# Kernel optimization log

Hardware: AMD Instinct MI355X
Metric: run time of the kernel (lower is better)

## Reference

```python
import jax, jax.numpy as jnp
import numpy as np

N_NODES = 50000
N_EDGES = 1200000
N_OD = 10000
D_NODE = 16
D_EDGE = 8
HID = 64
N_LAYERS = 3
K_MIN = 1.0
K_MAX = 50.0


def setup_inputs() -> dict:
    key = jax.random.key(0)
    ks = jax.random.split(key, 24)
    s = 0.05
    inp = {
        "node_features": jax.random.normal(ks[0], (N_NODES, D_NODE), jnp.float32),
        "edge_index": jax.random.randint(ks[1], (2, N_EDGES), 0, N_NODES, jnp.int32),
        "edge_features": jax.random.normal(ks[2], (N_EDGES, D_EDGE), jnp.float32),
        "od_pairs": jax.random.randint(ks[3], (2, N_OD), 0, N_NODES, jnp.int32),
        "traffic_stats": jax.random.normal(ks[4], (4,), jnp.float32),
        # projections
        "Wn": jax.random.normal(ks[5], (D_NODE, HID), jnp.float32) * s,
        "bn": jnp.zeros((HID,), jnp.float32),
        "We": jax.random.normal(ks[6], (D_EDGE, HID), jnp.float32) * s,
        "be": jnp.zeros((HID,), jnp.float32),
        # stacked GNN layer weights: message MLP on [h_src, e], update MLP on [h, agg]
        "Wm": jax.random.normal(ks[7], (N_LAYERS, 2 * HID, HID), jnp.float32) * s,
        "bm": jnp.zeros((N_LAYERS, HID), jnp.float32),
        "Wu": jax.random.normal(ks[8], (N_LAYERS, 2 * HID, HID), jnp.float32) * s,
        "bu": jnp.zeros((N_LAYERS, HID), jnp.float32),
        # per-flow score MLP on [h_src, h_dst]
        "Ws1": jax.random.normal(ks[9], (2 * HID, HID), jnp.float32) * s,
        "bs1": jnp.zeros((HID,), jnp.float32),
        "Ws2": jax.random.normal(ks[10], (HID, 1), jnp.float32) * s,
        "bs2": jnp.zeros((1,), jnp.float32),
        # DynamicKHead: Linear(HID+4,32) -> ReLU -> Linear(32,16) -> ReLU -> Linear(16,1)
        "Wk1": jax.random.normal(ks[11], (HID + 4, 32), jnp.float32) * s,
        "bk1": jnp.zeros((32,), jnp.float32),
        "Wk2": jax.random.normal(ks[12], (32, 16), jnp.float32) * s,
        "bk2": jnp.zeros((16,), jnp.float32),
        "Wk3": jax.random.normal(ks[13], (16, 1), jnp.float32) * s,
        "bk3": jnp.zeros((1,), jnp.float32),
    }
    return inp


def _forward(node_features, edge_features, traffic_stats,
             Wn, bn, We, be, Wm, bm, Wu, bu,
             Ws1, bs1, Ws2, bs2, Wk1, bk1, Wk2, bk2, Wk3, bk3,
             edge_index, od_pairs):
    relu = jax.nn.relu
    h = relu(node_features @ Wn + bn)          # [N, HID]
    e = relu(edge_features @ We + be)          # [E, HID]
    src, dst = edge_index[0], edge_index[1]
    for l in range(N_LAYERS):
        # gather-compute-scatter message passing with edge features
        m = relu(jnp.concatenate([h[src], e], axis=-1) @ Wm[l] + bm[l])  # [E, HID]
        agg = jax.ops.segment_sum(m, dst, num_segments=N_NODES)          # [N, HID]
        h = relu(jnp.concatenate([h, agg], axis=-1) @ Wu[l] + bu[l]) + h  # residual
    # per-flow scores from OD endpoint embeddings
    hp = jnp.concatenate([h[od_pairs[0]], h[od_pairs[1]]], axis=-1)      # [P, 2*HID]
    scores = (relu(hp @ Ws1 + bs1) @ Ws2 + bs2).squeeze(-1)              # [P]
    # dynamic-K head (dropout = identity in eval)
    graph_embed = h.mean(axis=0)                                          # [HID]
    x = jnp.concatenate([graph_embed, traffic_stats], axis=-1)
    raw = (relu(relu(x @ Wk1 + bk1) @ Wk2 + bk2) @ Wk3 + bk3).squeeze(-1)
    k_continuous = K_MIN + jax.nn.sigmoid(raw) * (K_MAX - K_MIN)
    return scores, k_continuous


def reference(node_features, edge_index, edge_features, od_pairs, traffic_stats,
              Wn, bn, We, be, Wm, bm, Wu, bu,
              Ws1, bs1, Ws2, bs2, Wk1, bk1, Wk2, bk2, Wk3, bk3):
    return _forward(node_features, edge_features, traffic_stats,
                    Wn, bn, We, be, Wm, bm, Wu, bu,
                    Ws1, bs1, Ws2, bs2, Wk1, bk1, Wk2, bk2, Wk3, bk3,
                    edge_index, od_pairs)
```

## Files before the change

kernel.cpp:

```cpp
#include <hip/hip_runtime.h>
#include <hip/hip_bf16.h>

#define OFF_WN   0
#define OFF_BN   1024
#define OFF_WE   1088
#define OFF_BE   1600
#define OFF_WM   1664
#define OFF_BM   26240
#define OFF_WU   26432
#define OFF_BU   51008
#define OFF_WS1  51200
#define OFF_BS1  59392
#define OFF_WS2  59456
#define OFF_BS2  59520
#define OFF_WK1  59521
#define OFF_BK1  61697
#define OFF_WK2  61729
#define OFF_BK2  62241
#define OFF_WK3  62257
#define OFF_BK3  62273
#define OFF_TS   62274
#define OFF_GSUM 62278
#define OFF_FLAG 62344
#define OFF_BSUM 62400
#define OFF_BOFF 62900
#define OFF_H    65536

typedef __attribute__((ext_vector_type(8))) short bfrag;
typedef __attribute__((ext_vector_type(4))) float ffrag;

__device__ __forceinline__ float bf2f(unsigned short u) {
    unsigned int i = ((unsigned int)u) << 16;
    float f;
    __builtin_memcpy(&f, &i, sizeof(f));
    return f;
}
__device__ __forceinline__ float bflo(unsigned int u) {
    unsigned int i = u << 16;
    float f; __builtin_memcpy(&f, &i, sizeof(f)); return f;
}
__device__ __forceinline__ float bfhi(unsigned int u) {
    unsigned int i = u & 0xffff0000u;
    float f; __builtin_memcpy(&f, &i, sizeof(f)); return f;
}
__device__ __forceinline__ unsigned int f2bf_rne(float f) {
    unsigned int u; __builtin_memcpy(&u, &f, 4);
    return (u + 0x7fffu + ((u >> 16) & 1u)) >> 16;
}
__device__ __forceinline__ unsigned int pack2bf(float a, float b) {
    return f2bf_rne(a) | (f2bf_rne(b) << 16);
}
__device__ __forceinline__ unsigned int cvt_pk_bf16(float a, float b) {
    unsigned int r;
    asm("v_cvt_pk_bf16_f32 %0, %1, %2" : "=v"(r) : "v"(a), "v"(b));
    return r;
}

__global__ void detect_dtype_kernel(const unsigned short* __restrict__ nf,
                                    int* __restrict__ flag) {
    int t = threadIdx.x;
    float m = 0.f;
    for (int i = t; i < 1024; i += 64) {
        float v = fabsf(bf2f(nf[i]));
        if (!isnan(v)) m = fmaxf(m, v);
        else m = 1e30f;
    }
    for (int o = 32; o > 0; o >>= 1) m = fmaxf(m, __shfl_down(m, o));
    if (t == 0) flag[0] = (m > 1e6f) ? 1 : 0;
}

struct ConvArgs {
    const void* src[19];
    int off[19];
    int n[19];
};

__global__ __launch_bounds__(256) void convert_all_kernel(
        ConvArgs a, float* __restrict__ ws, const int* __restrict__ flagp) {
    int isf32 = *flagp;
    int ai = blockIdx.y;
    int i  = blockIdx.x * blockDim.x + threadIdx.x;
    if (i < a.n[ai]) {
        float v = isf32 ? ((const float*)a.src[ai])[i]
                        : bf2f(((const unsigned short*)a.src[ai])[i]);
        ws[a.off[ai] + i] = v;
    }
}

__global__ __launch_bounds__(256) void wtrans_prep_kernel(
        const float* __restrict__ ws, short* __restrict__ Wb) {
    int idx = blockIdx.x * 256 + threadIdx.x;
    if (idx < 12288) {
        int l = idx >> 12, rem = idx & 4095, n = rem >> 6, k = rem & 63;
        Wb[idx] = (short)f2bf_rne(ws[OFF_WM + l * 8192 + 4096 + k * 64 + n]);
    } else if (idx < 24576) {
        int j = idx - 12288;
        int l = j >> 12, rem = j & 4095, n = rem >> 6, k = rem & 63;
        Wb[idx] = (short)f2bf_rne(ws[OFF_WM + l * 8192 + k * 64 + n]);
    } else if (idx < 49152) {
        int j = idx - 24576;
        int l = j >> 13, rem = j & 8191, n = rem >> 7, k = rem & 127;
        Wb[idx] = (short)f2bf_rne(ws[OFF_WU + l * 8192 + k * 64 + n]);
    } else if (idx < 51200) {
        int j = idx - 49152;
        int n = j >> 5, k = j & 31;
        Wb[idx] = (k < 8) ? (short)f2bf_rne(ws[OFF_WE + k * 64 + n]) : (short)0;
    } else if (idx < 59392) {
        int j = idx - 51200;
        int n = j >> 7, k = j & 127;
        Wb[idx] = (short)f2bf_rne(ws[OFF_WS1 + k * 64 + n]);
    }
}

__global__ __launch_bounds__(256) void node_proj_kernel(
        const void* __restrict__ nf, const float* __restrict__ ws,
        float* __restrict__ h, int N, const int* __restrict__ flagp) {
    int idx = blockIdx.x * blockDim.x + threadIdx.x;
    if (idx >= N * 64) return;
    int isf32 = *flagp;
    int i = idx >> 6, c = idx & 63;
    const float* Wn = ws + OFF_WN;
    float acc = ws[OFF_BN + c];
    float x[16];
    if (isf32) {
        const float* row = (const float*)nf + (size_t)i * 16;
#pragma unroll
        for (int k = 0; k < 16; ++k) x[k] = row[k];
    } else {
        const unsigned short* row = (const unsigned short*)nf + (size_t)i * 16;
#pragma unroll
        for (int k = 0; k < 16; ++k) x[k] = bf2f(row[k]);
    }
#pragma unroll
    for (int k = 0; k < 16; ++k) acc = fmaf(x[k], Wn[k * 64 + c], acc);
    h[idx] = fmaxf(acc, 0.f);
}

__global__ __launch_bounds__(256) void count_kernel(
        const int* __restrict__ dst, int* __restrict__ deg,
        int* __restrict__ rank, int E, int dorank) {
    int e = blockIdx.x * blockDim.x + threadIdx.x;
    if (e < E) {
        int r = atomicAdd(&deg[dst[e]], 1);
        if (dorank) rank[e] = r;
    }
}

__global__ __launch_bounds__(256) void scan_blocks_kernel(
        const int* __restrict__ deg, int* __restrict__ incl,
        int* __restrict__ bsum, int N) {
    int tid = threadIdx.x;
    int gid = blockIdx.x * 256 + tid;
    int v = (gid < N) ? deg[gid] : 0;
    int lane = tid & 63, w = tid >> 6;
    int x = v;
#pragma unroll
    for (int o = 1; o < 64; o <<= 1) {
        int y = __shfl_up(x, o);
        if (lane >= o) x += y;
    }
    __shared__ int wsum[4];
    __shared__ int woff[4];
    if (lane == 63) wsum[w] = x;
    __syncthreads();
    if (tid == 0) {
        int a = 0;
#pragma unroll
        for (int i = 0; i < 4; ++i) { woff[i] = a; a += wsum[i]; }
    }
    __syncthreads();
    x += woff[w];
    if (gid < N) incl[gid] = x;
    if (tid == 255) bsum[blockIdx.x] = x;
}

__global__ __launch_bounds__(256) void scan_bsum_kernel(
        const int* __restrict__ bsum, int* __restrict__ boff, int nb) {
    __shared__ int sh[256];
    int tid = threadIdx.x;
    int carry = 0;
    for (int base = 0; base < nb; base += 256) {
        int v = (base + tid < nb) ? bsum[base + tid] : 0;
        sh[tid] = v;
        __syncthreads();
        for (int o = 1; o < 256; o <<= 1) {
            int t = (tid >= o) ? sh[tid - o] : 0;
            __syncthreads();
            sh[tid] += t;
            __syncthreads();
        }
        if (base + tid < nb) boff[base + tid] = carry + sh[tid] - v;
        __syncthreads();
        carry += sh[255];
        __syncthreads();
    }
}

__global__ __launch_bounds__(256) void scan_finalize_kernel(
        const int* __restrict__ deg, const int* __restrict__ incl,
        const int* __restrict__ boff, int* __restrict__ out,
        int* __restrict__ cursor, int N, int tailval) {
    int gid = blockIdx.x * 256 + threadIdx.x;
    if (gid < N) {
        int ex = boff[blockIdx.x] + incl[gid] - deg[gid];
        out[gid] = ex;
        cursor[gid] = ex;
    }
    if (gid == 0) out[N] = tailval;
}

__global__ __launch_bounds__(256) void fill_kernel(
        const int* __restrict__ src, const int* __restrict__ dst,
        const void* __restrict__ ef, int* __restrict__ cursor,
        const int* __restrict__ rank, const int* __restrict__ off,
        int* __restrict__ eid, int* __restrict__ srcs,
        float* __restrict__ rec, int E, int big,
        const int* __restrict__ flagp) {
    int e = blockIdx.x * blockDim.x + threadIdx.x;
    if (e >= E) return;
    int d = dst[e];
    if (big) {
        int pos = off[d] + rank[e];
        unsigned p01, p23, p45, p67;
        if (*flagp) {
            const float4* p = (const float4*)ef + (size_t)e * 2;
            float4 a = p[0], b = p[1];
            p01 = pack2bf(a.x, a.y); p23 = pack2bf(a.z, a.w);
            p45 = pack2bf(b.x, b.y); p67 = pack2bf(b.z, b.w);
        } else {
            uint4 r = ((const uint4*)ef)[e];
            p01 = r.x; p23 = r.y; p45 = r.z; p67 = r.w;
        }
        float* o = rec + (size_t)pos * 6;
        *(uint2*)o       = make_uint2((unsigned)src[e], (unsigned)d);
        *(uint2*)(o + 2) = make_uint2(p01, p23);
        *(uint2*)(o + 4) = make_uint2(p45, p67);
    } else {
        int pos = atomicAdd(&cursor[d], 1);
        eid[pos] = e;
        srcs[pos] = src[e];
    }
}

__global__ __launch_bounds__(256) void spans_kernel(
        const int* __restrict__ off, int* __restrict__ spans, int N) {
    int i = blockIdx.x * blockDim.x + threadIdx.x;
    if (i >= N) return;
    int k0 = off[i], k1 = off[i + 1];
    spans[i] = (k1 > k0) ? (((k1 - 1) >> 6) - (k0 >> 6) + 1) : 0;
}

__global__ __launch_bounds__(256) void nodeA_mfma_kernel(
        const short* __restrict__ W1T, const float* __restrict__ bm,
        const float* __restrict__ h, float* __restrict__ A, int N) {
    __shared__ short lds_w[64 * 72];
    __shared__ short lds_x[4][64 * 72];
    const int tid = threadIdx.x, wid = tid >> 6, lane = tid & 63;
    const int r = lane & 15, q = lane >> 4;
    const int nb0 = blockIdx.x * 256 + wid * 64;

#pragma unroll
    for (int j = 0; j < 2; ++j) {
        int f8 = (tid * 2 + j) * 8;
        int row = f8 >> 6, k = f8 & 63;
        *(uint4*)&lds_w[row * 72 + k] = ((const uint4*)W1T)[tid * 2 + j];
    }
    short* xt = &lds_x[wid][0];
#pragma unroll 1
    for (int it = 0; it < 16; ++it) {
        int f4 = it * 64 + lane;
        int node = f4 >> 4, c4 = f4 & 15;
        int gn = nb0 + node; if (gn >= N) gn = N - 1;
        float4 v = ((const float4*)h)[(size_t)gn * 16 + c4];
        *(uint2*)&xt[node * 72 + c4 * 4] =
            make_uint2(pack2bf(v.x, v.y), pack2bf(v.z, v.w));
    }
    __syncthreads();

    bfrag bg[4][2];
#pragma unroll
    for (int ni = 0; ni < 4; ++ni)
#pragma unroll
        for (int ki = 0; ki < 2; ++ki)
            bg[ni][ki] = *(const bfrag*)&lds_w[(ni * 16 + r) * 72 + ki * 32 + q * 8];
    float buv[4];
#pragma unroll
    for (int ni = 0; ni < 4; ++ni) buv[ni] = bm[ni * 16 + r];

    ffrag C[4][4];
#pragma unroll
    for (int mi = 0; mi < 4; ++mi) {
        bfrag af[2];
#pragma unroll
        for (int ki = 0; ki < 2; ++ki)
            af[ki] = *(const bfrag*)&xt[(mi * 16 + r) * 72 + ki * 32 + q * 8];
#pragma unroll
        for (int ni = 0; ni < 4; ++ni) {
            ffrag c = {buv[ni], buv[ni], buv[ni], buv[ni]};
            c = __builtin_amdgcn_mfma_f32_16x16x32_bf16(af[0], bg[ni][0], c, 0, 0, 0);
            c = __builtin_amdgcn_mfma_f32_16x16x32_bf16(af[1], bg[ni][1], c, 0, 0, 0);
            C[mi][ni] = c;
        }
    }
#pragma unroll
    for (int mi = 0; mi < 4; ++mi)
#pragma unroll
        for (int rr = 0; rr < 4; ++rr) {
            int gn = nb0 + mi * 16 + q * 4 + rr;
            if (gn < N) {
#pragma unroll
                for (int ni = 0; ni < 4; ++ni)
                    A[(size_t)gn * 64 + ni * 16 + r] = C[mi][ni][rr];
            }
        }
}

__global__ __launch_bounds__(256, 4) void msg_mfma_red(
        const short* __restrict__ WeT, const float* __restrict__ be,
        const short* __restrict__ WbT, const float* __restrict__ rec,
        const float* __restrict__ A, float* __restrict__ pbuf,
        const int* __restrict__ off, const int* __restrict__ pstart, int E) {
    __shared__ short lds_ev[4][64 * 72];
    __shared__ int   lds_src[4][64];
    const int tid = threadIdx.x;
    const int wid = tid >> 6, lane = tid & 63;
    const int w = blockIdx.x * 4 + wid;
    if (w * 64 >= E) return;
    const int slot = w * 64 + lane;
    const int slotc = (slot < E) ? slot : (E - 1);

    const float* rbase = rec + (size_t)slotc * 6;
    uint2 u0 = *(const uint2*)rbase;
    uint2 u1 = *(const uint2*)(rbase + 2);
    uint2 u2 = *(const uint2*)(rbase + 4);
    int s  = (int)u0.x;
    int di = (int)u0.y;
    int pstv = pstart[di];
    int offv = off[di];
    lds_src[wid][lane] = s;

    short* evb = &lds_ev[wid][0];
    short* evrow = evb + lane * 72;
    *(uint4*)(evrow) = make_uint4(u1.x, u1.y, u2.x, u2.y);
    uint4 z4 = make_uint4(0u, 0u, 0u, 0u);
    *(uint4*)(evrow + 8)  = z4;
    *(uint4*)(evrow + 16) = z4;
    *(uint4*)(evrow + 24) = z4;

    const int r = lane & 15, q = lane >> 4;

    bfrag afe[4];
#pragma unroll
    for (int mi = 0; mi < 4; ++mi)
        afe[mi] = *(const bfrag*)(evb + (mi * 16 + r) * 72 + q * 8);

#pragma unroll
    for (int ni = 0; ni < 4; ++ni) {
        bfrag bge = *(const bfrag*)(WeT + (ni * 16 + r) * 32 + q * 8);
        float4 b4 = *(const float4*)(be + ni * 16 + q * 4);
#pragma unroll
        for (int mi = 0; mi < 4; ++mi) {
            ffrag c = {b4.x, b4.y, b4.z, b4.w};
            c = __builtin_amdgcn_mfma_f32_16x16x32_bf16(bge, afe[mi], c, 0, 0, 0);
            unsigned lo = cvt_pk_bf16(fmaxf(c[0], 0.f), fmaxf(c[1], 0.f));
            unsigned hi = cvt_pk_bf16(fmaxf(c[2], 0.f), fmaxf(c[3], 0.f));
            *(uint2*)(evb + (mi * 16 + r) * 72 + ni * 16 + q * 4) =
                make_uint2(lo, hi);
        }
    }

    bfrag af[4][2];
#pragma unroll
    for (int mi = 0; mi < 4; ++mi)
#pragma unroll
        for (int ki = 0; ki < 2; ++ki)
            af[mi][ki] = *(const bfrag*)(evb + (mi * 16 + r) * 72 + ki * 32 + q * 8);

    const float* ap[4][4];
#pragma unroll
    for (int mi = 0; mi < 4; ++mi) {
        int4 sr = *(const int4*)&lds_src[wid][mi * 16 + q * 4];
        ap[mi][0] = A + (size_t)sr.x * 64 + r;
        ap[mi][1] = A + (size_t)sr.y * 64 + r;
        ap[mi][2] = A + (size_t)sr.z * 64 + r;
        ap[mi][3] = A + (size_t)sr.w * 64 + r;
    }

#pragma unroll
    for (int ni = 0; ni < 4; ++ni) {
        bfrag bg0 = *(const bfrag*)(WbT + (ni * 16 + r) * 64 + q * 8);
        bfrag bg1 = *(const bfrag*)(WbT + (ni * 16 + r) * 64 + 32 + q * 8);
        ffrag C[4];
#pragma unroll
        for (int mi = 0; mi < 4; ++mi) {
            C[mi][0] = ap[mi][0][ni * 16];
            C[mi][1] = ap[mi][1][ni * 16];
            C[mi][2] = ap[mi][2][ni * 16];
            C[mi][3] = ap[mi][3][ni * 16];
        }
#pragma unroll
        for (int mi = 0; mi < 4; ++mi) {
            C[mi] = __builtin_amdgcn_mfma_f32_16x16x32_bf16(af[mi][0], bg0, C[mi], 0, 0, 0);
            C[mi] = __builtin_amdgcn_mfma_f32_16x16x32_bf16(af[mi][1], bg1, C[mi], 0, 0, 0);
        }
#pragma unroll
        for (int mi = 0; mi < 4; ++mi) {
            unsigned lo = cvt_pk_bf16(fmaxf(C[mi][0], 0.f), fmaxf(C[mi][1], 0.f));
            unsigned hi = cvt_pk_bf16(fmaxf(C[mi][2], 0.f), fmaxf(C[mi][3], 0.f));
            *(uint2*)(evb + (ni * 16 + r) * 72 + mi * 16 + q * 4) =
                make_uint2(lo, hi);
        }
    }

    int kmax = E - w * 64; if (kmax > 64) kmax = 64;
    if (kmax < 64) {
        for (int k = kmax; k < 64; ++k) evb[lane * 72 + k] = 0;
    }
    int prevd = __shfl_up(di, 1);
    unsigned long long sm = __ballot(lane != 0 && di != prevd);
    int curp = __shfl(pstv, 0) + (w - (__shfl(offv, 0) >> 6));
    float acc = 0.f;
#pragma unroll
    for (int g = 0; g < 8; ++g) {
        uint4 v = *(const uint4*)(evb + lane * 72 + g * 8);
        float f0 = bflo(v.x), f1 = bfhi(v.x), f2 = bflo(v.y), f3 = bfhi(v.y);
        float f4 = bflo(v.z), f5 = bfhi(v.z), f6 = bflo(v.w), f7 = bfhi(v.w);
        unsigned gm = (unsigned)(sm >> (g * 8)) & 0xffu;
        if (gm == 0) {
            acc += (((f0 + f1) + (f2 + f3)) + ((f4 + f5) + (f6 + f7)));
        } else {
            float fv[8] = {f0, f1, f2, f3, f4, f5, f6, f7};
#pragma unroll
            for (int j = 0; j < 8; ++j) {
                if (gm & (1u << j)) {
                    pbuf[(size_t)curp * 64 + lane] = acc;
                    acc = 0.f;
                    curp = __shfl(pstv, g * 8 + j);
                }
                acc += fv[j];
            }
        }
    }
    pbuf[(size_t)curp * 64 + lane] = acc;
}

__global__ __launch_bounds__(256) void fixup_kernel(
        const float* __restrict__ pbuf, const int* __restrict__ off,
        const int* __restrict__ pstart, float* __restrict__ agg, int N) {
    int tid = blockIdx.x * blockDim.x + threadIdx.x;
    int i = tid >> 2, q = tid & 3;
    if (i >= N) return;
    int k0 = off[i], k1 = off[i + 1];
    float acc[16];
#pragma unroll
    for (int c = 0; c < 16; ++c) acc[c] = 0.f;
    if (k1 > k0) {
        int nsp = ((k1 - 1) >> 6) - (k0 >> 6) + 1;
        int p = pstart[i];
        for (int j = 0; j < nsp; ++j) {
            const float4* pr = (const float4*)(pbuf + (size_t)(p + j) * 64 + q * 16);
#pragma unroll
            for (int c = 0; c < 4; ++c) {
                float4 v = pr[c];
                acc[4 * c] += v.x; acc[4 * c + 1] += v.y;
                acc[4 * c + 2] += v.z; acc[4 * c + 3] += v.w;
            }
        }
    }
    float4* o4 = (float4*)(agg + (size_t)i * 64 + q * 16);
#pragma unroll
    for (int c = 0; c < 4; ++c)
        o4[c] = make_float4(acc[4 * c], acc[4 * c + 1], acc[4 * c + 2], acc[4 * c + 3]);
}

__global__ __launch_bounds__(128) void update_mfma_kernel(
        const short* __restrict__ WuT, const float* __restrict__ bu,
        float* __restrict__ h, const float* __restrict__ agg, int N) {
    __shared__ short lds_w[64 * 136];
    __shared__ short lds_x[2][64 * 136];
    const int tid = threadIdx.x, wid = tid >> 6, lane = tid & 63;
    const int r = lane & 15, q = lane >> 4;
    const int nb0 = blockIdx.x * 128 + wid * 64;
#pragma unroll
    for (int j = 0; j < 8; ++j) {
        int f8 = (tid * 8 + j) * 8;
        int row = f8 >> 7, k = f8 & 127;
        *(uint4*)&lds_w[row * 136 + k] = ((const uint4*)WuT)[tid * 8 + j];
    }
    short* xt = &lds_x[wid][0];
#pragma unroll 1
    for (int it = 0; it < 32; ++it) {
        int f4 = it * 64 + lane;
        int node = f4 >> 5, c4 = f4 & 31;
        int gn = nb0 + node; if (gn >= N) gn = N - 1;
        const float4* src = (c4 < 16)
            ? ((const float4*)h + (size_t)gn * 16 + c4)
            : ((const float4*)agg + (size_t)gn * 16 + (c4 - 16));
        float4 v = *src;
        *(uint2*)&xt[node * 136 + c4 * 4] =
            make_uint2(pack2bf(v.x, v.y), pack2bf(v.z, v.w));
    }
    __syncthreads();
    bfrag bg[4][4];
#pragma unroll
    for (int ni = 0; ni < 4; ++ni)
#pragma unroll
        for (int ki = 0; ki < 4; ++ki)
            bg[ni][ki] = *(const bfrag*)&lds_w[(ni * 16 + r) * 136 + ki * 32 + q * 8];
    float buv[4];
#pragma unroll
    for (int ni = 0; ni < 4; ++ni) buv[ni] = bu[ni * 16 + r];
    ffrag C[4][4];
#pragma unroll
    for (int mi = 0; mi < 4; ++mi) {
        bfrag af[4];
#pragma unroll
        for (int ki = 0; ki < 4; ++ki)
            af[ki] = *(const bfrag*)&xt[(mi * 16 + r) * 136 + ki * 32 + q * 8];
#pragma unroll
        for (int ni = 0; ni < 4; ++ni) {
            ffrag c = {buv[ni], buv[ni], buv[ni], buv[ni]};
#pragma unroll
            for (int ki = 0; ki < 4; ++ki)
                c = __builtin_amdgcn_mfma_f32_16x16x32_bf16(af[ki], bg[ni][ki], c, 0, 0, 0);
            C[mi][ni] = c;
        }
    }
#pragma unroll
    for (int mi = 0; mi < 4; ++mi)
#pragma unroll
        for (int rr = 0; rr < 4; ++rr) {
            int nl = mi * 16 + q * 4 + rr;
            int gn = nb0 + nl;
            if (gn < N) {
#pragma unroll
                for (int ni = 0; ni < 4; ++ni) {
                    float hold = bf2f((unsigned short)xt[nl * 136 + ni * 16 + r]);
                    h[(size_t)gn * 64 + ni * 16 + r] =
                        fmaxf(C[mi][ni][rr], 0.f) + hold;
                }
            }
        }
}

__global__ __launch_bounds__(256) void gather_msg_fallback(
        const float* __restrict__ Wm2, const float* __restrict__ We,
        const float* __restrict__ be, const void* __restrict__ ef,
        const int* __restrict__ srcs, const int* __restrict__ eid,
        const int* __restrict__ off, const float* __restrict__ A,
        float* __restrict__ agg, int N, const int* __restrict__ flagp) {
    int i = blockIdx.x * blockDim.x + threadIdx.x;
    if (i >= N) return;
    int isf32 = *flagp;
    int k0 = off[i], k1 = off[i + 1];
    float acc[64];
#pragma unroll
    for (int c = 0; c < 64; ++c) acc[c] = 0.f;
    for (int k = k0; k < k1; ++k) {
        int s = srcs[k];
        int e = eid[k];
        const float4* a4 = (const float4*)(A + (size_t)s * 64);
        float t[64];
#pragma unroll
        for (int c = 0; c < 16; ++c) {
            float4 v = a4[c];
            t[4 * c] = v.x; t[4 * c + 1] = v.y; t[4 * c + 2] = v.z; t[4 * c + 3] = v.w;
        }
        float efv[8];
        if (isf32) {
            const float4* e4 = (const float4*)ef + (size_t)e * 2;
            float4 ra = e4[0], rb = e4[1];
            efv[0]=ra.x; efv[1]=ra.y; efv[2]=ra.z; efv[3]=ra.w;
            efv[4]=rb.x; efv[5]=rb.y; efv[6]=rb.z; efv[7]=rb.w;
        } else {
            uint4 rr = ((const uint4*)ef)[e];
            efv[0]=bflo(rr.x); efv[1]=bfhi(rr.x); efv[2]=bflo(rr.y); efv[3]=bfhi(rr.y);
            efv[4]=bflo(rr.z); efv[5]=bfhi(rr.z); efv[6]=bflo(rr.w); efv[7]=bfhi(rr.w);
        }
#pragma unroll 1
        for (int d0 = 0; d0 < 64; d0 += 8) {
            float ev[8];
#pragma unroll
            for (int dd = 0; dd < 8; ++dd) {
                float a = be[d0 + dd];
#pragma unroll
                for (int kk = 0; kk < 8; ++kk) a = fmaf(efv[kk], We[kk * 64 + d0 + dd], a);
                ev[dd] = fmaxf(a, 0.f);
            }
#pragma unroll
            for (int dd = 0; dd < 8; ++dd) {
                const float* w = Wm2 + (d0 + dd) * 64;
#pragma unroll
                for (int c = 0; c < 64; ++c) t[c] = fmaf(ev[dd], w[c], t[c]);
            }
        }
#pragma unroll
        for (int c = 0; c < 64; ++c) acc[c] += fmaxf(t[c], 0.f);
    }
    float4* o4 = (float4*)(agg + (size_t)i * 64);
#pragma unroll
    for (int c = 0; c < 16; ++c)
        o4[c] = make_float4(acc[4 * c], acc[4 * c + 1], acc[4 * c + 2], acc[4 * c + 3]);
}

__global__ __launch_bounds__(128) void scores_mfma_kernel(
        const short* __restrict__ Ws1T, const float* __restrict__ bs1,
        const float* __restrict__ Ws2, const float* __restrict__ bs2,
        const int* __restrict__ ods, const int* __restrict__ odd,
        const float* __restrict__ h, void* __restrict__ out, int P,
        const int* __restrict__ flagp) {
    __shared__ short lds_w[64 * 136];
    __shared__ short lds_x[2][64 * 136];
    const int tid = threadIdx.x, wid = tid >> 6, lane = tid & 63;
    const int r = lane & 15, q = lane >> 4;
    const int pb0 = blockIdx.x * 128 + wid * 64;
#pragma unroll
    for (int j = 0; j < 8; ++j) {
        int f8 = (tid * 8 + j) * 8;
        int row = f8 >> 7, k = f8 & 127;
        *(uint4*)&lds_w[row * 136 + k] = ((const uint4*)Ws1T)[tid * 8 + j];
    }
    short* xt = &lds_x[wid][0];
#pragma unroll 1
    for (int it = 0; it < 32; ++it) {
        int f4 = it * 64 + lane;
        int pr = f4 >> 5, c4 = f4 & 31;
        int gp = pb0 + pr; if (gp >= P) gp = P - 1;
        int node = (c4 < 16) ? ods[gp] : odd[gp];
        int cc = (c4 < 16) ? c4 : (c4 - 16);
        float4 v = ((const float4*)h)[(size_t)node * 16 + cc];
        *(uint2*)&xt[pr * 136 + c4 * 4] =
            make_uint2(pack2bf(v.x, v.y), pack2bf(v.z, v.w));
    }
    __syncthreads();

    bfrag bg[4][4];
#pragma unroll
    for (int ni = 0; ni < 4; ++ni)
#pragma unroll
        for (int ki = 0; ki < 4; ++ki)
            bg[ni][ki] = *(const bfrag*)&lds_w[(ni * 16 + r) * 136 + ki * 32 + q * 8];
    float buv[4], w2v[4];
#pragma unroll
    for (int ni = 0; ni < 4; ++ni) { buv[ni] = bs1[ni * 16 + r]; w2v[ni] = Ws2[ni * 16 + r]; }
    int isf32 = *flagp;
    float b2 = bs2[0];

#pragma unroll
    for (int mi = 0; mi < 4; ++mi) {
        bfrag af[4];
#pragma unroll
        for (int ki = 0; ki < 4; ++ki)
            af[ki] = *(const bfrag*)&xt[(mi * 16 + r) * 136 + ki * 32 + q * 8];
        float part[4] = {0.f, 0.f, 0.f, 0.f};
#pragma unroll
        for (int ni = 0; ni < 4; ++ni) {
            ffrag c = {buv[ni], buv[ni], buv[ni], buv[ni]};
#pragma unroll
            for (int ki = 0; ki < 4; ++ki)
                c = __builtin_amdgcn_mfma_f32_16x16x32_bf16(af[ki], bg[ni][ki], c, 0, 0, 0);
#pragma unroll
            for (int rr = 0; rr < 4; ++rr)
                part[rr] = fmaf(fmaxf(c[rr], 0.f), w2v[ni], part[rr]);
        }
#pragma unroll
        for (int rr = 0; rr < 4; ++rr) {
            float v = part[rr];
            v += __shfl_xor(v, 1); v += __shfl_xor(v, 2);
            v += __shfl_xor(v, 4); v += __shfl_xor(v, 8);
            if (r == 0) {
                int p = pb0 + mi * 16 + q * 4 + rr;
                if (p < P) {
                    float score = v + b2;
                    if (isf32) ((float*)out)[p] = score;
                    else ((__hip_bfloat16*)out)[p] = __float2bfloat16(score);
                }
            }
        }
    }
}

__global__ __launch_bounds__(256) void embed_kernel(
        const float* __restrict__ h, float* __restrict__ gsum, int N) {
    __shared__ float red[256];
    int c = threadIdx.x & 63;
    int sub = threadIdx.x >> 6;
    float a = 0.f;
    for (int i = blockIdx.x * 4 + sub; i < N; i += gridDim.x * 4)
        a += h[(size_t)i * 64 + c];
    red[threadIdx.x] = a;
    __syncthreads();
    if (threadIdx.x < 64) {
        float t = red[threadIdx.x] + red[threadIdx.x + 64] +
                  red[threadIdx.x + 128] + red[threadIdx.x + 192];
        unsafeAtomicAdd(&gsum[threadIdx.x], t);
    }
}

__global__ void khead_kernel(const float* __restrict__ ws,
                             void* __restrict__ out, int N, int P,
                             const int* __restrict__ flagp) {
    if (threadIdx.x != 0 || blockIdx.x != 0) return;
    float x[68];
    float invN = 1.f / (float)N;
#pragma unroll
    for (int c = 0; c < 64; ++c) x[c] = ws[OFF_GSUM + c] * invN;
#pragma unroll
    for (int k = 0; k < 4; ++k) x[64 + k] = ws[OFF_TS + k];
    float h1[32];
    for (int j = 0; j < 32; ++j) {
        float a = ws[OFF_BK1 + j];
        for (int i = 0; i < 68; ++i) a = fmaf(x[i], ws[OFF_WK1 + i * 32 + j], a);
        h1[j] = fmaxf(a, 0.f);
    }
    float h2[16];
    for (int k2 = 0; k2 < 16; ++k2) {
        float a = ws[OFF_BK2 + k2];
        for (int j = 0; j < 32; ++j) a = fmaf(h1[j], ws[OFF_WK2 + j * 16 + k2], a);
        h2[k2] = fmaxf(a, 0.f);
    }
    float raw = ws[OFF_BK3];
    for (int k2 = 0; k2 < 16; ++k2) raw = fmaf(h2[k2], ws[OFF_WK3 + k2], raw);
    float sig = 1.f / (1.f + expf(-raw));
    float k = 1.f + 49.f * sig;
    if (*flagp) ((float*)out)[P] = k;
    else ((__hip_bfloat16*)out)[P] = __float2bfloat16(k);
}

extern "C" void kernel_launch(void* const* d_in, const int* in_sizes, int n_in,
                              void* d_out, int out_size, void* d_ws, size_t ws_size,
                              hipStream_t stream) {
    const void* nf = d_in[0];
    const int*  ei = (const int*)d_in[1];
    const void* ef = d_in[2];
    const int*  od = (const int*)d_in[3];
    float* ws = (float*)d_ws;

    const int N = in_sizes[0] / 16;
    const int E = in_sizes[1] / 2;
    const int P = in_sizes[3] / 2;

    float* h      = ws + OFF_H;
    float* agg    = h + (size_t)N * 64;
    float* A      = agg + (size_t)N * 64;
    int*   deg    = (int*)(A + (size_t)N * 64);
    int*   off    = deg + N;
    int*   cursor = off + N + 1;
    int*   pstart = cursor + N;
    int*   eid    = pstart + N + 1;
    int*   srcs   = eid + E;
    short* WbT    = (short*)(srcs + E);
    short* W1T    = WbT + 12288;
    short* WuT    = WbT + 24576;
    short* WeT    = WbT + 49152;
    short* Ws1T   = WbT + 51200;
    int*   rank   = (int*)(WbT + 59392);
    int*   flag   = (int*)(ws + OFF_FLAG);
    int*   bsum   = (int*)(ws + OFF_BSUM);
    int*   boff   = (int*)(ws + OFF_BOFF);

    size_t fsofar = (size_t)OFF_H + 3 * (size_t)N * 64
                  + (size_t)(N + (N + 1) + N + (N + 1) + E + E + E) + 29696;
    size_t recOff = (fsofar + 7) & ~(size_t)7;
    float* rec = ws + recOff;
    size_t pbufOff = recOff + (size_t)E * 6;
    float* pbuf = ws + pbufOff;
    long pbufRows = (long)N + E / 64 + 128;
    size_t needBytes = (pbufOff + (size_t)pbufRows * 64) * sizeof(float);
    const bool big = (ws_size >= needBytes);

    const int* srcv = ei;
    const int* dstv = ei + E;

    detect_dtype_kernel<<<1, 64, 0, stream>>>((const unsigned short*)nf, flag);

    ConvArgs ca;
    const int srcidx[19] = {5, 6, 7, 8, 9, 10, 11, 12, 13, 14, 15, 16, 17, 18, 19, 20, 21, 22, 4};
    const int wsoff[19]  = {OFF_WN, OFF_BN, OFF_WE, OFF_BE, OFF_WM, OFF_BM, OFF_WU, OFF_BU,
                            OFF_WS1, OFF_BS1, OFF_WS2, OFF_BS2, OFF_WK1, OFF_BK1, OFF_WK2,
                            OFF_BK2, OFF_WK3, OFF_BK3, OFF_TS};
    int maxn = 0;
    for (int i = 0; i < 19; ++i) {
        ca.src[i] = d_in[srcidx[i]];
        ca.off[i] = wsoff[i];
        ca.n[i]   = in_sizes[srcidx[i]];
        if (ca.n[i] > maxn) maxn = ca.n[i];
    }
    dim3 cgrid((maxn + 255) / 256, 19);
    convert_all_kernel<<<cgrid, 256, 0, stream>>>(ca, ws, flag);
    wtrans_prep_kernel<<<232, 256, 0, stream>>>(ws, WbT);

    node_proj_kernel<<<(N * 64 + 255) / 256, 256, 0, stream>>>(nf, ws, h, N, flag);

    hipMemsetAsync(deg, 0, (size_t)N * sizeof(int), stream);
    count_kernel<<<(E + 255) / 256, 256, 0, stream>>>(dstv, deg, rank, E, big ? 1 : 0);
    int nb = (N + 255) / 256;
    scan_blocks_kernel<<<nb, 256, 0, stream>>>(deg, cursor, bsum, N);
    scan_bsum_kernel<<<1, 256, 0, stream>>>(bsum, boff, nb);
    scan_finalize_kernel<<<nb, 256, 0, stream>>>(deg, cursor, boff, off, cursor, N, E);
    fill_kernel<<<(E + 255) / 256, 256, 0, stream>>>(
        srcv, dstv, ef, cursor, rank, off, eid, srcs, rec, E, big ? 1 : 0, flag);

    if (big) {
        spans_kernel<<<nb, 256, 0, stream>>>(off, deg, N);
        scan_blocks_kernel<<<nb, 256, 0, stream>>>(deg, cursor, bsum, N);
        scan_bsum_kernel<<<1, 256, 0, stream>>>(bsum, boff, nb);
        scan_finalize_kernel<<<nb, 256, 0, stream>>>(deg, cursor, boff, pstart, cursor, N, 0);
    }

    const int N4 = N * 4;
    const int mblocks = (E + 255) / 256;
    const int ablocks = (N + 255) / 256;
    const int ublocks = (N + 127) / 128;
    for (int l = 0; l < 3; ++l) {
        nodeA_mfma_kernel<<<ablocks, 256, 0, stream>>>(
            W1T + l * 4096, ws + OFF_BM + l * 64, h, A, N);
        if (big) {
            msg_mfma_red<<<mblocks, 256, 0, stream>>>(
                WeT, ws + OFF_BE, WbT + l * 4096, rec, A, pbuf, off, pstart, E);
            fixup_kernel<<<(N4 + 255) / 256, 256, 0, stream>>>(
                pbuf, off, pstart, agg, N);
        } else {
            const float* Wm2 = ws + OFF_WM + l * 8192 + 4096;
            gather_msg_fallback<<<(N + 255) / 256, 256, 0, stream>>>(
                Wm2, ws + OFF_WE, ws + OFF_BE, ef, srcs, eid, off, A, agg, N, flag);
        }
        update_mfma_kernel<<<ublocks, 128, 0, stream>>>(
            WuT + l * 8192, ws + OFF_BU + l * 64, h, agg, N);
    }

    scores_mfma_kernel<<<(P + 127) / 128, 128, 0, stream>>>(
        Ws1T, ws + OFF_BS1, ws + OFF_WS2, ws + OFF_BS2,
        od, od + P, h, d_out, P, flag);

    hipMemsetAsync(ws + OFF_GSUM, 0, 64 * sizeof(float), stream);
    embed_kernel<<<256, 256, 0, stream>>>(h, ws + OFF_GSUM, N);
    khead_kernel<<<1, 64, 0, stream>>>(ws, d_out, N, P, flag);
}
```

Measured before the change: 621.8 us.

## Replace sorted edge records with index pairs and gather edge features in message kernel

The fill kernel now writes only an (edge id, src) pair per sorted slot, and a separate kernel converts edge features to bf16 in original edge order. The message kernel then gathers dst and the edge features through the edge id instead of reading a contiguous 24-byte sorted record. This makes the one-time scatter in fill cheaper, but each of the three layers now does random gathers of dst and 16-byte features. The khead kernel is also parallelised across a wavefront instead of running on a single thread.

```diff
diff --git a/kernel.cpp b/kernel.cpp
--- a/kernel.cpp
+++ b/kernel.cpp
@@ -211,35 +211,38 @@
 
 __global__ __launch_bounds__(256) void fill_kernel(
         const int* __restrict__ src, const int* __restrict__ dst,
-        const void* __restrict__ ef, int* __restrict__ cursor,
+        int* __restrict__ cursor,
         const int* __restrict__ rank, const int* __restrict__ off,
         int* __restrict__ eid, int* __restrict__ srcs,
-        float* __restrict__ rec, int E, int big,
-        const int* __restrict__ flagp) {
+        uint2* __restrict__ esb, int E, int big) {
     int e = blockIdx.x * blockDim.x + threadIdx.x;
     if (e >= E) return;
     int d = dst[e];
     if (big) {
         int pos = off[d] + rank[e];
-        unsigned p01, p23, p45, p67;
-        if (*flagp) {
-            const float4* p = (const float4*)ef + (size_t)e * 2;
-            float4 a = p[0], b = p[1];
-            p01 = pack2bf(a.x, a.y); p23 = pack2bf(a.z, a.w);
-            p45 = pack2bf(b.x, b.y); p67 = pack2bf(b.z, b.w);
-        } else {
-            uint4 r = ((const uint4*)ef)[e];
-            p01 = r.x; p23 = r.y; p45 = r.z; p67 = r.w;
-        }
-        float* o = rec + (size_t)pos * 6;
-        *(uint2*)o       = make_uint2((unsigned)src[e], (unsigned)d);
-        *(uint2*)(o + 2) = make_uint2(p01, p23);
-        *(uint2*)(o + 4) = make_uint2(p45, p67);
+        esb[pos] = make_uint2((unsigned)e, (unsigned)src[e]);
     } else {
         int pos = atomicAdd(&cursor[d], 1);
         eid[pos] = e;
         srcs[pos] = src[e];
     }
+}
+
+__global__ __launch_bounds__(256) void efb_kernel(
+        const void* __restrict__ ef, uint4* __restrict__ efb, int E,
+        const int* __restrict__ flagp) {
+    int e = blockIdx.x * blockDim.x + threadIdx.x;
+    if (e >= E) return;
+    uint4 v;
+    if (*flagp) {
+        const float4* p = (const float4*)ef + (size_t)e * 2;
+        float4 a = p[0], b = p[1];
+        v = make_uint4(pack2bf(a.x, a.y), pack2bf(a.z, a.w),
+                       pack2bf(b.x, b.y), pack2bf(b.z, b.w));
+    } else {
+        v = ((const uint4*)ef)[e];
+    }
+    efb[e] = v;
 }
 
 __global__ __launch_bounds__(256) void spans_kernel(
@@ -317,7 +320,8 @@
 
 __global__ __launch_bounds__(256, 4) void msg_mfma_red(
         const short* __restrict__ WeT, const float* __restrict__ be,
-        const short* __restrict__ WbT, const float* __restrict__ rec,
+        const short* __restrict__ WbT, const uint2* __restrict__ esb,
+        const int* __restrict__ dstv, const uint4* __restrict__ efb,
         const float* __restrict__ A, float* __restrict__ pbuf,
         const int* __restrict__ off, const int* __restrict__ pstart, int E) {
     __shared__ short lds_ev[4][64 * 72];
@@ -329,19 +333,17 @@
     const int slot = w * 64 + lane;
     const int slotc = (slot < E) ? slot : (E - 1);
 
-    const float* rbase = rec + (size_t)slotc * 6;
-    uint2 u0 = *(const uint2*)rbase;
-    uint2 u1 = *(const uint2*)(rbase + 2);
-    uint2 u2 = *(const uint2*)(rbase + 4);
-    int s  = (int)u0.x;
-    int di = (int)u0.y;
+    uint2 es = esb[slotc];
+    int e  = (int)es.x;
+    int s  = (int)es.y;
+    int di = dstv[e];
     int pstv = pstart[di];
     int offv = off[di];
     lds_src[wid][lane] = s;
 
     short* evb = &lds_ev[wid][0];
     short* evrow = evb + lane * 72;
-    *(uint4*)(evrow) = make_uint4(u1.x, u1.y, u2.x, u2.y);
+    *(uint4*)(evrow) = efb[e];
     uint4 z4 = make_uint4(0u, 0u, 0u, 0u);
     *(uint4*)(evrow + 8)  = z4;
     *(uint4*)(evrow + 16) = z4;
@@ -700,31 +702,34 @@
 __global__ void khead_kernel(const float* __restrict__ ws,
                              void* __restrict__ out, int N, int P,
                              const int* __restrict__ flagp) {
-    if (threadIdx.x != 0 || blockIdx.x != 0) return;
-    float x[68];
+    __shared__ float sh1[32];
+    __shared__ float sh2[16];
+    int lane = threadIdx.x;
     float invN = 1.f / (float)N;
-#pragma unroll
-    for (int c = 0; c < 64; ++c) x[c] = ws[OFF_GSUM + c] * invN;
-#pragma unroll
-    for (int k = 0; k < 4; ++k) x[64 + k] = ws[OFF_TS + k];
-    float h1[32];
+    float a1 = (lane < 32) ? ws[OFF_BK1 + lane] : 0.f;
+#pragma unroll
+    for (int i = 0; i < 68; ++i) {
+        float xi = (i < 64) ? ws[OFF_GSUM + i] * invN : ws[OFF_TS + i - 64];
+        if (lane < 32) a1 = fmaf(xi, ws[OFF_WK1 + i * 32 + lane], a1);
+    }
+    if (lane < 32) sh1[lane] = fmaxf(a1, 0.f);
+    __syncthreads();
+    float a2 = (lane < 16) ? ws[OFF_BK2 + lane] : 0.f;
+#pragma unroll
     for (int j = 0; j < 32; ++j) {
-        float a = ws[OFF_BK1 + j];
-        for (int i = 0; i < 68; ++i) a = fmaf(x[i], ws[OFF_WK1 + i * 32 + j], a);
-        h1[j] = fmaxf(a, 0.f);
-    }
-    float h2[16];
-    for (int k2 = 0; k2 < 16; ++k2) {
-        float a = ws[OFF_BK2 + k2];
-        for (int j = 0; j < 32; ++j) a = fmaf(h1[j], ws[OFF_WK2 + j * 16 + k2], a);
-        h2[k2] = fmaxf(a, 0.f);
-    }
-    float raw = ws[OFF_BK3];
-    for (int k2 = 0; k2 < 16; ++k2) raw = fmaf(h2[k2], ws[OFF_WK3 + k2], raw);
-    float sig = 1.f / (1.f + expf(-raw));
-    float k = 1.f + 49.f * sig;
-    if (*flagp) ((float*)out)[P] = k;
-    else ((__hip_bfloat16*)out)[P] = __float2bfloat16(k);
+        if (lane < 16) a2 = fmaf(sh1[j], ws[OFF_WK2 + j * 16 + lane], a2);
+    }
+    if (lane < 16) sh2[lane] = fmaxf(a2, 0.f);
+    __syncthreads();
+    if (lane == 0) {
+        float raw = ws[OFF_BK3];
+#pragma unroll
+        for (int k2 = 0; k2 < 16; ++k2) raw = fmaf(sh2[k2], ws[OFF_WK3 + k2], raw);
+        float sig = 1.f / (1.f + expf(-raw));
+        float k = 1.f + 49.f * sig;
+        if (*flagp) ((float*)out)[P] = k;
+        else ((__hip_bfloat16*)out)[P] = __float2bfloat16(k);
+    }
 }
 
 extern "C" void kernel_launch(void* const* d_in, const int* in_sizes, int n_in,
@@ -761,9 +766,11 @@
 
     size_t fsofar = (size_t)OFF_H + 3 * (size_t)N * 64
                   + (size_t)(N + (N + 1) + N + (N + 1) + E + E + E) + 29696;
-    size_t recOff = (fsofar + 7) & ~(size_t)7;
-    float* rec = ws + recOff;
-    size_t pbufOff = recOff + (size_t)E * 6;
+    size_t recOff = (fsofar + 3) & ~(size_t)3;
+    uint2* esb = (uint2*)(ws + recOff);
+    size_t efbOff = recOff + (((size_t)E * 2 + 3) & ~(size_t)3);
+    uint4* efb = (uint4*)(ws + efbOff);
+    size_t pbufOff = efbOff + (size_t)E * 4;
     float* pbuf = ws + pbufOff;
     long pbufRows = (long)N + E / 64 + 128;
     size_t needBytes = (pbufOff + (size_t)pbufRows * 64) * sizeof(float);
@@ -799,7 +806,10 @@
     scan_bsum_kernel<<<1, 256, 0, stream>>>(bsum, boff, nb);
     scan_finalize_kernel<<<nb, 256, 0, stream>>>(deg, cursor, boff, off, cursor, N, E);
     fill_kernel<<<(E + 255) / 256, 256, 0, stream>>>(
-        srcv, dstv, ef, cursor, rank, off, eid, srcs, rec, E, big ? 1 : 0, flag);
+        srcv, dstv, cursor, rank, off, eid, srcs, esb, E, big ? 1 : 0);
+    if (big) {
+        efb_kernel<<<(E + 255) / 256, 256, 0, stream>>>(ef, efb, E, flag);
+    }
 
     if (big) {
         spans_kernel<<<nb, 256, 0, stream>>>(off, deg, N);
@@ -817,7 +827,8 @@
             W1T + l * 4096, ws + OFF_BM + l * 64, h, A, N);
         if (big) {
             msg_mfma_red<<<mblocks, 256, 0, stream>>>(
-                WeT, ws + OFF_BE, WbT + l * 4096, rec, A, pbuf, off, pstart, E);
+                WeT, ws + OFF_BE, WbT + l * 4096, esb, dstv, efb, A, pbuf,
+                off, pstart, E);
             fixup_kernel<<<(N4 + 255) / 256, 256, 0, stream>>>(
                 pbuf, off, pstart, agg, N);
         } else {
```

New measurement: 630.1 us. About the same (+1.3%).
